# Kernel optimization log

Measured on AMD Instinct MI355X. Metric: run time of the kernel, lower is better.

The kernel has to match this reference:

```python
import jax, jax.numpy as jnp
import numpy as np

B, D_IN, R, D_P, K, D_C, ITERS = 4096, 2048, 7, 128, 25, 16, 3


def _ln(x, g, b, eps=1e-5):
    m = jnp.mean(x, axis=-1, keepdims=True)
    v = jnp.var(x, axis=-1, keepdims=True)
    return (x - m) * jax.lax.rsqrt(v + eps) * g + b


def _squash(x):
    eps = 1e-6
    ns = jnp.sum(x * x, axis=-1, keepdims=True)
    scale = ns / jnp.maximum(1.0 + ns, eps)
    return scale * x / (jnp.sqrt(ns) + eps)


def setup_inputs() -> dict:
    key = jax.random.key(0)
    ks = jax.random.split(key, 8)
    f = lambda k, shp, s=0.02: (jax.random.normal(k, shp) * s).astype(jnp.float32)
    return {
        "z": jax.random.normal(ks[0], (B, D_IN), jnp.float32),
        "W_prim": f(ks[1], (D_IN, R * D_P)),
        "b_prim": jnp.zeros((R * D_P,), jnp.float32),
        "ln_a_g": jnp.ones((D_IN,), jnp.float32),
        "ln_a_b": jnp.zeros((D_IN,), jnp.float32),
        "W_act": f(ks[2], (D_IN, R)),
        "b_act": jnp.zeros((R,), jnp.float32),
        "w_caps": (np.sqrt(K / (D_P * R)).astype(np.float32)
                   * jax.random.normal(ks[3], (R, D_P, K, D_C))).astype(jnp.float32),
        "ln_c_g": jnp.ones((D_C,), jnp.float32),
        "ln_c_b": jnp.zeros((D_C,), jnp.float32),
        "beta_u": f(ks[4], (K,), 1.0),
        "ln_h_g": jnp.ones((R * D_C,), jnp.float32),
        "ln_h_b": jnp.zeros((R * D_C,), jnp.float32),
        "W_h1": f(ks[5], (R * D_C, 4 * R * D_C)),
        "b_h1": jnp.zeros((4 * R * D_C,), jnp.float32),
        "W_h2": f(ks[6], (4 * R * D_C, 1)),
        "b_h2": jnp.zeros((1,), jnp.float32),
    }


def reference(z, W_prim, b_prim, ln_a_g, ln_a_b, W_act, b_act, w_caps,
              ln_c_g, ln_c_b, beta_u, ln_h_g, ln_h_b, W_h1, b_h1, W_h2, b_h2):
    # primary capsules: [B, R, D_P] poses + [B, R] activations
    pose = _squash((z @ W_prim + b_prim).reshape(B, R, D_P))
    act = jnp.clip(jax.nn.sigmoid(_ln(z, ln_a_g, ln_a_b) @ W_act + b_act), 0.0, 1.0)

    # votes: [B, R, K, D_C]
    u = jnp.einsum('brd,rdkh->brkh', pose, w_caps)
    scale = 1.0 / np.sqrt(D_C).astype(np.float32)

    # iterative routing (EM/softmax-agreement style)
    q = jnp.full((B, R, K), 1.0 / K, dtype=z.dtype)
    class_pose = None
    for _ in range(ITERS):
        wts = q * act[:, :, None]                               # [B,R,K]
        class_pose = _ln(jnp.einsum('brk,brkh->bkh', wts, u), ln_c_g, ln_c_b)
        agree = jnp.einsum('bkh,brkh->brk', class_pose, u) * scale
        q = jax.nn.softmax(agree, axis=-1)

    class_act = jax.nn.sigmoid(beta_u[None, :] + jnp.einsum('brk,br->bk', q, act))
    route_class_emb = q[..., None] * u                          # [B,R,K,D_C]

    # concat per-route interaction vectors -> [B, K, R*D_C]
    class_embed = jnp.transpose(route_class_emb, (0, 2, 1, 3)).reshape(B, K, R * D_C)
    h = jax.nn.gelu(_ln(class_embed, ln_h_g, ln_h_b) @ W_h1 + b_h1, approximate=False)
    logits = (h @ W_h2 + b_h2)[..., 0]                          # [B, K]

    return (logits, class_embed, class_pose, class_act, q, pose, act, route_class_emb)
```

## Files before the change

### kernel.cpp

```cpp
#include <hip/hip_runtime.h>
#include <cstddef>

#define BB 4096
#define DIN 2048
#define RR 7
#define DP 128
#define KK 25
#define DC 16
#define NITERS 3
#define RKH (RR*KK*DC)
#define RK  (RR*KK)
#define KH  (KK*DC)
#define HD  (RR*DC)
#define H4  (4*HD)

typedef __attribute__((ext_vector_type(8))) short bf16x8;
typedef __attribute__((ext_vector_type(4))) float f32x4;

__device__ __forceinline__ unsigned pk_bf16(float a, float b) {
    union { float f; unsigned u; } xa, xb;
    xa.f = a; xb.f = b;
    unsigned ua = (xa.u + 0x7FFFu + ((xa.u >> 16) & 1u)) >> 16;
    unsigned ub = (xb.u + 0x7FFFu + ((xb.u >> 16) & 1u)) >> 16;
    return (ua & 0xFFFFu) | (ub << 16);
}

__device__ __forceinline__ float gelu_tanh(float x) {
    float x3 = x * x * x;
    float tt = 0.7978845608f * (x + 0.044715f * x3);
    float e = __expf(2.0f * tt);
    float th = 1.0f - 2.0f / (e + 1.0f);
    return 0.5f * x * (1.0f + th);
}

__global__ __launch_bounds__(256) void transpose_cvt_kernel(
    const float* __restrict__ src, unsigned short* __restrict__ dst, int RS, int CS)
{
    __shared__ float T[64][65];
    int r0 = blockIdx.x * 64, c0 = blockIdx.y * 64;
    size_t bo = (size_t)blockIdx.z * RS * CS;
    src += bo; dst += bo;
    int t = threadIdx.x;
    for (int s = t; s < 64 * 16; s += 256) {
        int row = s >> 4, c4 = s & 15;
        int gr = r0 + row, gc = c0 + c4 * 4;
        float4 v = make_float4(0.f, 0.f, 0.f, 0.f);
        if (gr < RS && gc < CS) v = *(const float4*)(src + (size_t)gr * CS + gc);
        T[row][c4 * 4 + 0] = v.x; T[row][c4 * 4 + 1] = v.y;
        T[row][c4 * 4 + 2] = v.z; T[row][c4 * 4 + 3] = v.w;
    }
    __syncthreads();
    for (int s = t; s < 64 * 16; s += 256) {
        int col = s >> 4, r4 = s & 15;
        int gc = c0 + col, gr = r0 + r4 * 4;
        if (gc < CS && gr + 3 < RS) {
            unsigned lo = pk_bf16(T[r4 * 4 + 0][col], T[r4 * 4 + 1][col]);
            unsigned hi = pk_bf16(T[r4 * 4 + 2][col], T[r4 * 4 + 3][col]);
            *(uint2*)(dst + (size_t)gc * RS + gr) = make_uint2(lo, hi);
        }
    }
}

__global__ __launch_bounds__(256) void act_kernel(
    const float* __restrict__ z, const float* __restrict__ g, const float* __restrict__ bb,
    const float* __restrict__ Wa, const float* __restrict__ ba,
    float* __restrict__ act_out)
{
    int b = blockIdx.x;
    int t = threadIdx.x;
    __shared__ float zs[DIN];
    __shared__ float ws1[4], ws2[4];
    __shared__ float wr[4][RR];
    const float* zr = z + (size_t)b * DIN;
    float s = 0.f, s2 = 0.f;
    for (int i = t; i < DIN; i += 256) {
        float v = zr[i]; zs[i] = v; s += v; s2 += v * v;
    }
    for (int off = 32; off; off >>= 1) { s += __shfl_down(s, off); s2 += __shfl_down(s2, off); }
    int w = t >> 6, lane = t & 63;
    if (lane == 0) { ws1[w] = s; ws2[w] = s2; }
    __syncthreads();
    s  = ws1[0] + ws1[1] + ws1[2] + ws1[3];
    s2 = ws2[0] + ws2[1] + ws2[2] + ws2[3];
    float mean = s * (1.0f / DIN);
    float var  = s2 * (1.0f / DIN) - mean * mean;
    float rstd = rsqrtf(var + 1e-5f);
    float acc[RR];
#pragma unroll
    for (int r = 0; r < RR; ++r) acc[r] = 0.f;
    for (int i = t; i < DIN; i += 256) {
        float y = (zs[i] - mean) * rstd * g[i] + bb[i];
#pragma unroll
        for (int r = 0; r < RR; ++r) acc[r] += y * Wa[i * RR + r];
    }
    for (int off = 32; off; off >>= 1) {
#pragma unroll
        for (int r = 0; r < RR; ++r) acc[r] += __shfl_down(acc[r], off);
    }
    if (lane == 0) {
#pragma unroll
        for (int r = 0; r < RR; ++r) wr[w][r] = acc[r];
    }
    __syncthreads();
    if (t < RR) {
        float v = wr[0][t] + wr[1][t] + wr[2][t] + wr[3][t] + ba[t];
        float sg = 1.0f / (1.0f + expf(-v));
        sg = fminf(fmaxf(sg, 0.0f), 1.0f);
        act_out[(size_t)b * RR + t] = sg;
    }
}

__global__ __launch_bounds__(256) void pose_mfma(
    const float* __restrict__ z, const unsigned short* __restrict__ WpT,
    const float* __restrict__ bp, float* __restrict__ pose_out)
{
    __shared__ __align__(16) unsigned short As[128 * 40];
    __shared__ __align__(16) unsigned short Bs[128 * 40];
    __shared__ float sq[2][128];
    int m0 = blockIdx.x * 128, r = blockIdx.y, t = threadIdx.x;
    int n0 = r * DP;
    int w = t >> 6, l = t & 63;
    int lrow = l & 15, koff = l >> 4;
    int rbase = (w >> 1) * 64, cbase = (w & 1) * 64;
    f32x4 acc[4][4];
#pragma unroll
    for (int i = 0; i < 4; ++i)
#pragma unroll
        for (int j = 0; j < 4; ++j) acc[i][j] = 0.0f;
    for (int kt = 0; kt < DIN; kt += 32) {
#pragma unroll
        for (int q = 0; q < 4; ++q) {
            int s = t + 256 * q;
            int row = s >> 3, k4 = s & 7;
            float4 v = *(const float4*)(z + (size_t)(m0 + row) * DIN + kt + k4 * 4);
            *(uint2*)(As + row * 40 + k4 * 4) = make_uint2(pk_bf16(v.x, v.y), pk_bf16(v.z, v.w));
        }
#pragma unroll
        for (int q = 0; q < 2; ++q) {
            int s = t + 256 * q;
            int col = s >> 2, k8 = s & 3;
            uint4 v = *(const uint4*)(WpT + (size_t)(n0 + col) * DIN + kt + k8 * 8);
            *(uint4*)(Bs + col * 40 + k8 * 8) = v;
        }
        __syncthreads();
        bf16x8 a[4], b[4];
#pragma unroll
        for (int i = 0; i < 4; ++i)
            a[i] = *(const bf16x8*)(As + (rbase + i * 16 + lrow) * 40 + koff * 8);
#pragma unroll
        for (int j = 0; j < 4; ++j)
            b[j] = *(const bf16x8*)(Bs + (cbase + j * 16 + lrow) * 40 + koff * 8);
#pragma unroll
        for (int i = 0; i < 4; ++i)
#pragma unroll
            for (int j = 0; j < 4; ++j)
                acc[i][j] = __builtin_amdgcn_mfma_f32_16x16x32_bf16(a[i], b[j], acc[i][j], 0, 0, 0);
        __syncthreads();
    }
    float bpv[4];
#pragma unroll
    for (int j = 0; j < 4; ++j) bpv[j] = bp[n0 + cbase + j * 16 + lrow];
    float ns_[4][4];
#pragma unroll
    for (int i = 0; i < 4; ++i)
#pragma unroll
        for (int reg = 0; reg < 4; ++reg) {
            float ss = 0.f;
#pragma unroll
            for (int j = 0; j < 4; ++j) {
                float x = acc[i][j][reg] + bpv[j];
                acc[i][j][reg] = x;
                ss += x * x;
            }
            ss += __shfl_xor(ss, 1); ss += __shfl_xor(ss, 2);
            ss += __shfl_xor(ss, 4); ss += __shfl_xor(ss, 8);
            ns_[i][reg] = ss;
        }
    if (lrow == 0) {
#pragma unroll
        for (int i = 0; i < 4; ++i)
#pragma unroll
            for (int reg = 0; reg < 4; ++reg)
                sq[w & 1][rbase + i * 16 + koff * 4 + reg] = ns_[i][reg];
    }
    __syncthreads();
#pragma unroll
    for (int i = 0; i < 4; ++i)
#pragma unroll
        for (int reg = 0; reg < 4; ++reg) {
            int rl = rbase + i * 16 + koff * 4 + reg;
            float ns = sq[0][rl] + sq[1][rl];
            float factor = (ns / fmaxf(1.0f + ns, 1e-6f)) / (sqrtf(ns) + 1e-6f);
            size_t rowbase = ((size_t)(m0 + rl) * RR + r) * DP;
#pragma unroll
            for (int j = 0; j < 4; ++j)
                pose_out[rowbase + cbase + j * 16 + lrow] = acc[i][j][reg] * factor;
        }
}

__global__ __launch_bounds__(256) void votes_mfma(
    const float* __restrict__ pose, const unsigned short* __restrict__ wcT,
    float* __restrict__ u_out)
{
    __shared__ __align__(16) unsigned short As[128 * 152];
    __shared__ __align__(16) unsigned short Bs[80 * 152];
    int m0 = blockIdx.x * 128, r = blockIdx.y, n0 = blockIdx.z * 80;
    int t = threadIdx.x;
    int w = t >> 6, l = t & 63;
    int lrow = l & 15, koff = l >> 4;
    int rbase = w * 32;
#pragma unroll
    for (int q = 0; q < 16; ++q) {
        int s = t + 256 * q;
        int row = s >> 5, k4 = s & 31;
        float4 v = *(const float4*)(pose + ((size_t)(m0 + row) * RR + r) * DP + k4 * 4);
        *(uint2*)(As + row * 152 + k4 * 4) = make_uint2(pk_bf16(v.x, v.y), pk_bf16(v.z, v.w));
    }
    const unsigned short* wr_ = wcT + (size_t)r * KH * DP;
#pragma unroll
    for (int q = 0; q < 5; ++q) {
        int s = t + 256 * q;
        int col = s >> 4, k8 = s & 15;
        uint4 v = *(const uint4*)(wr_ + (size_t)(n0 + col) * DP + k8 * 8);
        *(uint4*)(Bs + col * 152 + k8 * 8) = v;
    }
    __syncthreads();
    f32x4 acc[2][5];
#pragma unroll
    for (int i = 0; i < 2; ++i)
#pragma unroll
        for (int j = 0; j < 5; ++j) acc[i][j] = 0.0f;
#pragma unroll
    for (int ks = 0; ks < 4; ++ks) {
        bf16x8 a[2], b[5];
#pragma unroll
        for (int i = 0; i < 2; ++i)
            a[i] = *(const bf16x8*)(As + (rbase + i * 16 + lrow) * 152 + ks * 32 + koff * 8);
#pragma unroll
        for (int j = 0; j < 5; ++j)
            b[j] = *(const bf16x8*)(Bs + (j * 16 + lrow) * 152 + ks * 32 + koff * 8);
#pragma unroll
        for (int i = 0; i < 2; ++i)
#pragma unroll
            for (int j = 0; j < 5; ++j)
                acc[i][j] = __builtin_amdgcn_mfma_f32_16x16x32_bf16(a[i], b[j], acc[i][j], 0, 0, 0);
    }
#pragma unroll
    for (int i = 0; i < 2; ++i)
#pragma unroll
        for (int reg = 0; reg < 4; ++reg) {
            int row = m0 + rbase + i * 16 + koff * 4 + reg;
            size_t base = ((size_t)row * RR + r) * KH + n0;
#pragma unroll
            for (int j = 0; j < 5; ++j)
                u_out[base + j * 16 + lrow] = acc[i][j][reg];
        }
}

__global__ __launch_bounds__(64) void routing_kernel(
    const float* __restrict__ u_in, const float* __restrict__ act_in,
    const float* __restrict__ lncg, const float* __restrict__ lncb,
    const float* __restrict__ beta_u,
    float* __restrict__ q_out, float* __restrict__ cp_out,
    float* __restrict__ ca_out, float* __restrict__ rce_out,
    float* __restrict__ ce_out)
{
    __shared__ __align__(16) float U[RKH];
    __shared__ float Q[RK];
    __shared__ float CP[KH];
    __shared__ float AG[RK];
    __shared__ float A7[RR];
    int b = blockIdx.x, t = threadIdx.x;
    const float4* u4 = (const float4*)(u_in + (size_t)b * RKH);
    float4* U4 = (float4*)U;
    for (int p = t; p < RKH / 4; p += 64) U4[p] = u4[p];
    if (t < RR) A7[t] = act_in[(size_t)b * RR + t];
    for (int p = t; p < RK; p += 64) Q[p] = 1.0f / KK;
    __syncthreads();
    for (int it = 0; it < NITERS; ++it) {
        for (int p = t; p < KH; p += 64) {
            int k = p / DC;
            float s = 0.f;
#pragma unroll
            for (int r = 0; r < RR; ++r) s += Q[r * KK + k] * A7[r] * U[r * KH + p];
            CP[p] = s;
        }
        __syncthreads();
        if (t < KK) {
            float m = 0.f;
#pragma unroll
            for (int h = 0; h < DC; ++h) m += CP[t * DC + h];
            m *= (1.0f / DC);
            float v = 0.f;
#pragma unroll
            for (int h = 0; h < DC; ++h) { float d = CP[t * DC + h] - m; v += d * d; }
            v *= (1.0f / DC);
            float rstd = rsqrtf(v + 1e-5f);
#pragma unroll
            for (int h = 0; h < DC; ++h)
                CP[t * DC + h] = (CP[t * DC + h] - m) * rstd * lncg[h] + lncb[h];
        }
        __syncthreads();
        for (int p = t; p < RK; p += 64) {
            int r = p / KK, k = p % KK;
            float s = 0.f;
#pragma unroll
            for (int h = 0; h < DC; ++h) s += CP[k * DC + h] * U[r * KH + k * DC + h];
            AG[p] = s * 0.25f;
        }
        __syncthreads();
        if (t < RR) {
            float mx = -1e30f;
            for (int k = 0; k < KK; ++k) mx = fmaxf(mx, AG[t * KK + k]);
            float e[KK], sum = 0.f;
            for (int k = 0; k < KK; ++k) { e[k] = expf(AG[t * KK + k] - mx); sum += e[k]; }
            float inv = 1.0f / sum;
            for (int k = 0; k < KK; ++k) Q[t * KK + k] = e[k] * inv;
        }
        __syncthreads();
    }
    if (t < KK) {
        float s = 0.f;
#pragma unroll
        for (int r = 0; r < RR; ++r) s += Q[r * KK + t] * A7[r];
        ca_out[(size_t)b * KK + t] = 1.0f / (1.0f + expf(-(beta_u[t] + s)));
    }
    for (int p = t; p < RK; p += 64) q_out[(size_t)b * RK + p] = Q[p];
    for (int p = t; p < KH; p += 64) cp_out[(size_t)b * KH + p] = CP[p];
    float4* rce4 = (float4*)(rce_out + (size_t)b * RKH);
    float4* ce4  = (float4*)ce_out;
    for (int p4 = t; p4 < RKH / 4; p4 += 64) {
        int base = p4 * 4;
        int r  = base / KH;
        int k  = (base % KH) / DC;
        int h0 = base % DC;
        float qv = Q[r * KK + k];
        float4 uv = U4[p4];
        float4 rv = make_float4(qv * uv.x, qv * uv.y, qv * uv.z, qv * uv.w);
        rce4[p4] = rv;
        size_t ci = ((size_t)b * RKH + (size_t)k * HD + (size_t)r * DC + h0) >> 2;
        ce4[ci] = rv;
    }
}

__global__ __launch_bounds__(256) void head_mfma(
    const float* __restrict__ ce, const float* __restrict__ g, const float* __restrict__ bb,
    const unsigned short* __restrict__ W1T, const float* __restrict__ b1,
    const float* __restrict__ W2, const float* __restrict__ b2,
    float* __restrict__ logits)
{
    __shared__ __align__(16) unsigned short As[128 * 152];
    __shared__ __align__(16) char pool[64 * 116 * 4];
    __shared__ float gbuf[HD], bbuf[HD];
    float* scr = (float*)pool;
    unsigned short* Bs = (unsigned short*)pool;
    unsigned* As32 = (unsigned*)As;
    unsigned* Bs32 = (unsigned*)Bs;
    int row0 = blockIdx.x * 128;
    int t = threadIdx.x;
    int w = t >> 6, l = t & 63;
    int lrow = l & 15, koff = l >> 4;
    if (t < HD) { gbuf[t] = g[t]; bbuf[t] = bb[t]; }
    for (int p = 0; p < 2; ++p) {
        for (int s = t; s < 64 * 28; s += 256) {
            int row = s / 28, q4 = s % 28;
            float4 v = *(const float4*)(ce + (size_t)(row0 + p * 64 + row) * HD + q4 * 4);
            *(float4*)(scr + row * 116 + q4 * 4) = v;
        }
        __syncthreads();
        {
            int tq = t & 3, row = t >> 2;
            float s1 = 0.f, s2 = 0.f;
            const float* rp = scr + row * 116 + tq * 28;
            for (int q = 0; q < 28; ++q) { float v = rp[q]; s1 += v; s2 += v * v; }
            s1 += __shfl_xor(s1, 1); s2 += __shfl_xor(s2, 1);
            s1 += __shfl_xor(s1, 2); s2 += __shfl_xor(s2, 2);
            float mean = s1 * (1.0f / HD);
            float var  = s2 * (1.0f / HD) - mean * mean;
            float rstd = rsqrtf(var + 1e-5f);
            int grow = p * 64 + row;
            for (int j = 0; j < 14; ++j) {
                int k = tq * 28 + 2 * j;
                float a = (rp[2 * j]     - mean) * rstd * gbuf[k]     + bbuf[k];
                float bv = (rp[2 * j + 1] - mean) * rstd * gbuf[k + 1] + bbuf[k + 1];
                As32[grow * 76 + tq * 14 + j] = pk_bf16(a, bv);
            }
        }
        __syncthreads();
    }
    for (int s = t; s < 128 * 8; s += 256) { int row = s >> 3; As32[row * 76 + 56 + (s & 7)] = 0; }
    for (int s = t; s < 64 * 8;  s += 256) { int col = s >> 3; Bs32[col * 76 + 56 + (s & 7)] = 0; }
    int rbase = w * 32;
    float logitAcc[2][4];
#pragma unroll
    for (int i = 0; i < 2; ++i)
#pragma unroll
        for (int reg = 0; reg < 4; ++reg) logitAcc[i][reg] = 0.f;
    for (int nc = 0; nc < 7; ++nc) {
        __syncthreads();
        for (int s = t; s < 64 * 14; s += 256) {
            int col = s / 14, k4 = s % 14;
            uint4 v = *(const uint4*)(W1T + (size_t)(nc * 64 + col) * HD + k4 * 8);
            *(uint4*)(Bs + col * 152 + k4 * 8) = v;
        }
        __syncthreads();
        f32x4 acc[2][4];
#pragma unroll
        for (int i = 0; i < 2; ++i)
#pragma unroll
            for (int j = 0; j < 4; ++j) acc[i][j] = 0.0f;
#pragma unroll
        for (int ks = 0; ks < 4; ++ks) {
            bf16x8 a[2], b[4];
#pragma unroll
            for (int i = 0; i < 2; ++i)
                a[i] = *(const bf16x8*)(As + (rbase + i * 16 + lrow) * 152 + ks * 32 + koff * 8);
#pragma unroll
            for (int j = 0; j < 4; ++j)
                b[j] = *(const bf16x8*)(Bs + (j * 16 + lrow) * 152 + ks * 32 + koff * 8);
#pragma unroll
            for (int i = 0; i < 2; ++i)
#pragma unroll
                for (int j = 0; j < 4; ++j)
                    acc[i][j] = __builtin_amdgcn_mfma_f32_16x16x32_bf16(a[i], b[j], acc[i][j], 0, 0, 0);
        }
        float b1v[4], w2v[4];
#pragma unroll
        for (int j = 0; j < 4; ++j) {
            b1v[j] = b1[nc * 64 + j * 16 + lrow];
            w2v[j] = W2[nc * 64 + j * 16 + lrow];
        }
#pragma unroll
        for (int i = 0; i < 2; ++i)
#pragma unroll
            for (int reg = 0; reg < 4; ++reg) {
                float sum = 0.f;
#pragma unroll
                for (int j = 0; j < 4; ++j) {
                    float x = acc[i][j][reg] + b1v[j];
                    sum += gelu_tanh(x) * w2v[j];
                }
                logitAcc[i][reg] += sum;
            }
    }
#pragma unroll
    for (int i = 0; i < 2; ++i)
#pragma unroll
        for (int reg = 0; reg < 4; ++reg) {
            float v = logitAcc[i][reg];
            v += __shfl_xor(v, 1); v += __shfl_xor(v, 2);
            v += __shfl_xor(v, 4); v += __shfl_xor(v, 8);
            logitAcc[i][reg] = v;
        }
    if (lrow == 0) {
        float b2v = b2[0];
#pragma unroll
        for (int i = 0; i < 2; ++i)
#pragma unroll
            for (int reg = 0; reg < 4; ++reg)
                logits[row0 + rbase + i * 16 + koff * 4 + reg] = logitAcc[i][reg] + b2v;
    }
}

__global__ __launch_bounds__(256) void pose_kernel(
    const float* __restrict__ z, const float* __restrict__ Wp, const float* __restrict__ bp,
    float* __restrict__ pose_out)
{
    __shared__ __align__(16) float As[64 * 36];
    __shared__ __align__(16) float Bs[32 * 128];
    int m0 = blockIdx.x * 64;
    int r  = blockIdx.y;
    int n0 = r * DP;
    int t  = threadIdx.x;
    int rg = t >> 5;
    int cg = t & 31;
    float acc[8][4] = {};
    for (int kt = 0; kt < DIN; kt += 32) {
#pragma unroll
        for (int q = 0; q < 2; ++q) {
            int s = t * 2 + q;
            int row = s >> 3, k4 = s & 7;
            float4 v = *(const float4*)(z + (size_t)(m0 + row) * DIN + kt + k4 * 4);
            *(float4*)(As + row * 36 + k4 * 4) = v;
        }
#pragma unroll
        for (int q = 0; q < 4; ++q) {
            int s = t + 256 * q;
            int row = s >> 5, c4 = s & 31;
            float4 v = *(const float4*)(Wp + (size_t)(kt + row) * (RR * DP) + n0 + c4 * 4);
            *(float4*)(Bs + row * 128 + c4 * 4) = v;
        }
        __syncthreads();
#pragma unroll
        for (int kk = 0; kk < 32; ++kk) {
            float4 bv = *(const float4*)(Bs + kk * 128 + cg * 4);
#pragma unroll
            for (int j = 0; j < 8; ++j) {
                float a = As[(rg * 8 + j) * 36 + kk];
                acc[j][0] += a * bv.x; acc[j][1] += a * bv.y;
                acc[j][2] += a * bv.z; acc[j][3] += a * bv.w;
            }
        }
        __syncthreads();
    }
    float bi0 = bp[n0 + cg * 4], bi1 = bp[n0 + cg * 4 + 1];
    float bi2 = bp[n0 + cg * 4 + 2], bi3 = bp[n0 + cg * 4 + 3];
#pragma unroll
    for (int j = 0; j < 8; ++j) {
        float x0 = acc[j][0] + bi0, x1 = acc[j][1] + bi1;
        float x2 = acc[j][2] + bi2, x3 = acc[j][3] + bi3;
        float ns = x0 * x0 + x1 * x1 + x2 * x2 + x3 * x3;
        for (int off = 1; off < 32; off <<= 1) ns += __shfl_xor(ns, off);
        float factor = (ns / fmaxf(1.0f + ns, 1e-6f)) / (sqrtf(ns) + 1e-6f);
        int row = m0 + rg * 8 + j;
        float4 o = make_float4(x0 * factor, x1 * factor, x2 * factor, x3 * factor);
        *(float4*)(pose_out + ((size_t)row * RR + r) * DP + cg * 4) = o;
    }
}

__global__ __launch_bounds__(256) void votes_kernel(
    const float* __restrict__ pose, const float* __restrict__ wc,
    float* __restrict__ u_out)
{
    __shared__ float As[64 * 129];
    __shared__ __align__(16) float Bs[64 * 80];
    int m0 = blockIdx.x * 64;
    int r  = blockIdx.y;
    int n0 = blockIdx.z * 80;
    int t  = threadIdx.x;
    const size_t wbase = (size_t)r * DP * KH;
#pragma unroll
    for (int q = 0; q < 8; ++q) {
        int s = t + 256 * q;
        int row = s >> 5, d4 = s & 31;
        float4 v = *(const float4*)(pose + ((size_t)(m0 + row) * RR + r) * DP + d4 * 4);
        As[row * 129 + d4 * 4 + 0] = v.x;
        As[row * 129 + d4 * 4 + 1] = v.y;
        As[row * 129 + d4 * 4 + 2] = v.z;
        As[row * 129 + d4 * 4 + 3] = v.w;
    }
    int m4 = t >> 4, n5 = t & 15;
    float acc[4][5];
#pragma unroll
    for (int i = 0; i < 4; ++i)
#pragma unroll
        for (int j = 0; j < 5; ++j) acc[i][j] = 0.f;
    for (int kt = 0; kt < DP; kt += 64) {
        __syncthreads();
#pragma unroll
        for (int q = 0; q < 5; ++q) {
            int s = t + 256 * q;
            int d = s / 20, c4 = s % 20;
            float4 v = *(const float4*)(wc + wbase + (size_t)(kt + d) * KH + n0 + c4 * 4);
            *(float4*)(Bs + d * 80 + c4 * 4) = v;
        }
        __syncthreads();
#pragma unroll 4
        for (int dd = 0; dd < 64; ++dd) {
            int d = kt + dd;
            float b_[5];
#pragma unroll
            for (int j = 0; j < 5; ++j) b_[j] = Bs[dd * 80 + n5 * 5 + j];
#pragma unroll
            for (int i = 0; i < 4; ++i) {
                float a = As[(m4 * 4 + i) * 129 + d];
#pragma unroll
                for (int j = 0; j < 5; ++j) acc[i][j] += a * b_[j];
            }
        }
    }
#pragma unroll
    for (int i = 0; i < 4; ++i) {
        int row = m0 + m4 * 4 + i;
        size_t base = ((size_t)row * RR + r) * KH + n0 + n5 * 5;
#pragma unroll
        for (int j = 0; j < 5; ++j) u_out[base + j] = acc[i][j];
    }
}

__global__ __launch_bounds__(256) void head_kernel(
    const float* __restrict__ ce, const float* __restrict__ g, const float* __restrict__ bb,
    const float* __restrict__ W1, const float* __restrict__ b1,
    const float* __restrict__ W2, const float* __restrict__ b2,
    float* __restrict__ logits)
{
    __shared__ __align__(16) float Y[64 * HD];
    __shared__ float Wc[HD * 64];
    __shared__ float Lg[64];
    int row0 = blockIdx.x * 64;
    int t = threadIdx.x;
    for (int s = t; s < 64 * HD; s += 256) Y[s] = ce[(size_t)row0 * HD + s];
    __syncthreads();
    if (t < 64) {
        float m = 0.f;
        for (int i = 0; i < HD; ++i) m += Y[t * HD + i];
        m *= (1.0f / HD);
        float v = 0.f;
        for (int i = 0; i < HD; ++i) { float d = Y[t * HD + i] - m; v += d * d; }
        v *= (1.0f / HD);
        float rstd = rsqrtf(v + 1e-5f);
        for (int i = 0; i < HD; ++i) Y[t * HD + i] = (Y[t * HD + i] - m) * rstd * g[i] + bb[i];
    }
    int rg = t >> 4;
    int cg = t & 15;
    float accRow[4] = {0.f, 0.f, 0.f, 0.f};
    for (int c0 = 0; c0 < H4; c0 += 64) {
        __syncthreads();
        for (int s = t; s < HD * 64; s += 256) {
            int i = s >> 6, c = s & 63;
            Wc[i * 64 + c] = W1[(size_t)i * H4 + c0 + c];
        }
        __syncthreads();
        float b1v[4], w2v[4];
#pragma unroll
        for (int c = 0; c < 4; ++c) { b1v[c] = b1[c0 + cg * 4 + c]; w2v[c] = W2[c0 + cg * 4 + c]; }
        float s_[4][4];
#pragma unroll
        for (int rr = 0; rr < 4; ++rr)
#pragma unroll
            for (int c = 0; c < 4; ++c) s_[rr][c] = b1v[c];
        for (int i4 = 0; i4 < HD / 4; ++i4) {
            float4 y4[4];
#pragma unroll
            for (int rr = 0; rr < 4; ++rr)
                y4[rr] = *(const float4*)(Y + (rg * 4 + rr) * HD + i4 * 4);
#pragma unroll
            for (int is = 0; is < 4; ++is) {
                float w_[4];
#pragma unroll
                for (int c = 0; c < 4; ++c) w_[c] = Wc[(i4 * 4 + is) * 64 + cg * 4 + c];
#pragma unroll
                for (int rr = 0; rr < 4; ++rr) {
                    float yv = (is == 0) ? y4[rr].x : (is == 1) ? y4[rr].y : (is == 2) ? y4[rr].z : y4[rr].w;
#pragma unroll
                    for (int c = 0; c < 4; ++c) s_[rr][c] += yv * w_[c];
                }
            }
        }
#pragma unroll
        for (int rr = 0; rr < 4; ++rr) {
#pragma unroll
            for (int c = 0; c < 4; ++c) {
                float x = s_[rr][c];
                float ge = 0.5f * x * (1.0f + erff(x * 0.70710678118654752440f));
                accRow[rr] += ge * w2v[c];
            }
        }
    }
#pragma unroll
    for (int rr = 0; rr < 4; ++rr) {
        float v = accRow[rr];
        v += __shfl_xor(v, 1); v += __shfl_xor(v, 2);
        v += __shfl_xor(v, 4); v += __shfl_xor(v, 8);
        if (cg == 0) Lg[rg * 4 + rr] = v;
    }
    __syncthreads();
    if (t < 64) logits[row0 + t] = Lg[t] + b2[0];
}

extern "C" void kernel_launch(void* const* d_in, const int* in_sizes, int n_in,
                              void* d_out, int out_size, void* d_ws, size_t ws_size,
                              hipStream_t stream) {
    const float* z    = (const float*)d_in[0];
    const float* Wp   = (const float*)d_in[1];
    const float* bp   = (const float*)d_in[2];
    const float* lnag = (const float*)d_in[3];
    const float* lnab = (const float*)d_in[4];
    const float* Wa   = (const float*)d_in[5];
    const float* ba   = (const float*)d_in[6];
    const float* wc   = (const float*)d_in[7];
    const float* lncg = (const float*)d_in[8];
    const float* lncb = (const float*)d_in[9];
    const float* beta = (const float*)d_in[10];
    const float* lnhg = (const float*)d_in[11];
    const float* lnhb = (const float*)d_in[12];
    const float* W1   = (const float*)d_in[13];
    const float* b1   = (const float*)d_in[14];
    const float* W2   = (const float*)d_in[15];
    const float* b2   = (const float*)d_in[16];

    float* out = (float*)d_out;
    float* o_logits = out;
    float* o_ce   = o_logits + (size_t)BB * KK;
    float* o_cp   = o_ce   + (size_t)BB * KK * HD;
    float* o_ca   = o_cp   + (size_t)BB * KK * DC;
    float* o_q    = o_ca   + (size_t)BB * KK;
    float* o_pose = o_q    + (size_t)BB * RK;
    float* o_act  = o_pose + (size_t)BB * RR * DP;
    float* o_rce  = o_act  + (size_t)BB * RR;

    const size_t WPT_ELE = (size_t)(RR * DP) * DIN;
    const size_t W1T_ELE = (size_t)H4 * HD;
    const size_t WCT_ELE = (size_t)RR * KH * DP;
    const size_t WS_NEED = (WPT_ELE + W1T_ELE + WCT_ELE) * sizeof(unsigned short);
    unsigned short* WpT = (unsigned short*)d_ws;
    unsigned short* W1T = WpT + WPT_ELE;
    unsigned short* wcT = W1T + W1T_ELE;

    hipLaunchKernelGGL(act_kernel, dim3(BB), dim3(256), 0, stream,
                       z, lnag, lnab, Wa, ba, o_act);

    if (ws_size >= WS_NEED) {
        hipLaunchKernelGGL(transpose_cvt_kernel, dim3(DIN / 64, (RR * DP) / 64, 1), dim3(256), 0, stream,
                           Wp, WpT, DIN, RR * DP);
        hipLaunchKernelGGL(transpose_cvt_kernel, dim3(2, 7, 1), dim3(256), 0, stream,
                           W1, W1T, HD, H4);
        hipLaunchKernelGGL(transpose_cvt_kernel, dim3(2, 7, RR), dim3(256), 0, stream,
                           wc, wcT, DP, KH);
        hipLaunchKernelGGL(pose_mfma, dim3(BB / 128, RR), dim3(256), 0, stream,
                           z, WpT, bp, o_pose);
        hipLaunchKernelGGL(votes_mfma, dim3(BB / 128, RR, 5), dim3(256), 0, stream,
                           o_pose, wcT, o_rce);
        hipLaunchKernelGGL(routing_kernel, dim3(BB), dim3(64), 0, stream,
                           o_rce, o_act, lncg, lncb, beta, o_q, o_cp, o_ca, o_rce, o_ce);
        hipLaunchKernelGGL(head_mfma, dim3(BB * KK / 128), dim3(256), 0, stream,
                           o_ce, lnhg, lnhb, W1T, b1, W2, b2, o_logits);
    } else {
        hipLaunchKernelGGL(pose_kernel, dim3(BB / 64, RR), dim3(256), 0, stream,
                           z, Wp, bp, o_pose);
        hipLaunchKernelGGL(votes_kernel, dim3(BB / 64, RR, 5), dim3(256), 0, stream,
                           o_pose, wc, o_rce);
        hipLaunchKernelGGL(routing_kernel, dim3(BB), dim3(64), 0, stream,
                           o_rce, o_act, lncg, lncb, beta, o_q, o_cp, o_ca, o_rce, o_ce);
        hipLaunchKernelGGL(head_kernel, dim3(BB * KK / 64), dim3(256), 0, stream,
                           o_ce, lnhg, lnhb, W1, b1, W2, b2, o_logits);
    }
}
```

Baseline: 387.4 us.

## Pre-swizzle W1 into MFMA fragment order and stage it once via LDS DMA

A new prep kernel writes W1 as bf16 laid out in MFMA fragment order, zero-padded to K=128. The head kernel loads the whole 448x128 weight block into LDS once with global_load_lds, removing the per-chunk barriers and the strided LDS loads. It also computes LayerNorm straight from registers into fragment-ordered A tiles held in registers, and caches b1/W2 in LDS. In exchange LDS use per block grows a lot (about 150KB), which lowers occupancy to one block per CU.

```diff
diff --git a/kernel.cpp b/kernel.cpp
--- a/kernel.cpp
+++ b/kernel.cpp
@@ -59,6 +59,21 @@
             *(uint2*)(dst + (size_t)gc * RS + gr) = make_uint2(lo, hi);
         }
     }
+}
+
+__global__ __launch_bounds__(256) void w1_frag_kernel(
+    const float* __restrict__ W1, unsigned short* __restrict__ W1F)
+{
+    int d = blockIdx.x * 256 + threadIdx.x;
+    int e2 = d & 3;
+    int lane = (d >> 2) & 63;
+    int fid = d >> 8;
+    int j = fid & 3, ks = (fid >> 2) & 3, nc = fid >> 4;
+    int col = nc * 64 + j * 16 + (lane & 15);
+    int k = ks * 32 + (lane >> 4) * 8 + e2 * 2;
+    float a = (k < HD)     ? W1[(size_t)k * H4 + col]       : 0.f;
+    float b = (k + 1 < HD) ? W1[(size_t)(k + 1) * H4 + col] : 0.f;
+    ((unsigned*)W1F)[d] = pk_bf16(a, b);
 }
 
 __global__ __launch_bounds__(256) void act_kernel(
@@ -345,65 +360,95 @@
 
 __global__ __launch_bounds__(256) void head_mfma(
     const float* __restrict__ ce, const float* __restrict__ g, const float* __restrict__ bb,
-    const unsigned short* __restrict__ W1T, const float* __restrict__ b1,
+    const unsigned short* __restrict__ W1F, const float* __restrict__ b1,
     const float* __restrict__ W2, const float* __restrict__ b2,
     float* __restrict__ logits)
 {
-    __shared__ __align__(16) unsigned short As[128 * 152];
-    __shared__ __align__(16) char pool[64 * 116 * 4];
-    __shared__ float gbuf[HD], bbuf[HD];
-    float* scr = (float*)pool;
-    unsigned short* Bs = (unsigned short*)pool;
-    unsigned* As32 = (unsigned*)As;
-    unsigned* Bs32 = (unsigned*)Bs;
+    __shared__ __align__(16) unsigned short As[128 * 128];
+    __shared__ __align__(16) unsigned short Bs[448 * 128];
+    __shared__ float LB1[H4];
+    __shared__ float LW2[H4];
     int row0 = blockIdx.x * 128;
     int t = threadIdx.x;
     int w = t >> 6, l = t & 63;
     int lrow = l & 15, koff = l >> 4;
-    if (t < HD) { gbuf[t] = g[t]; bbuf[t] = bb[t]; }
-    for (int p = 0; p < 2; ++p) {
-        for (int s = t; s < 64 * 28; s += 256) {
-            int row = s / 28, q4 = s % 28;
-            float4 v = *(const float4*)(ce + (size_t)(row0 + p * 64 + row) * HD + q4 * 4);
-            *(float4*)(scr + row * 116 + q4 * 4) = v;
-        }
-        __syncthreads();
-        {
-            int tq = t & 3, row = t >> 2;
-            float s1 = 0.f, s2 = 0.f;
-            const float* rp = scr + row * 116 + tq * 28;
-            for (int q = 0; q < 28; ++q) { float v = rp[q]; s1 += v; s2 += v * v; }
-            s1 += __shfl_xor(s1, 1); s2 += __shfl_xor(s2, 1);
-            s1 += __shfl_xor(s1, 2); s2 += __shfl_xor(s2, 2);
-            float mean = s1 * (1.0f / HD);
-            float var  = s2 * (1.0f / HD) - mean * mean;
-            float rstd = rsqrtf(var + 1e-5f);
-            int grow = p * 64 + row;
-            for (int j = 0; j < 14; ++j) {
-                int k = tq * 28 + 2 * j;
-                float a = (rp[2 * j]     - mean) * rstd * gbuf[k]     + bbuf[k];
-                float bv = (rp[2 * j + 1] - mean) * rstd * gbuf[k + 1] + bbuf[k + 1];
-                As32[grow * 76 + tq * 14 + j] = pk_bf16(a, bv);
-            }
-        }
-        __syncthreads();
-    }
-    for (int s = t; s < 128 * 8; s += 256) { int row = s >> 3; As32[row * 76 + 56 + (s & 7)] = 0; }
-    for (int s = t; s < 64 * 8;  s += 256) { int col = s >> 3; Bs32[col * 76 + 56 + (s & 7)] = 0; }
-    int rbase = w * 32;
+
+#pragma unroll
+    for (int q = 0; q < 28; ++q) {
+        int chunk = w * 28 + q;
+        __builtin_amdgcn_global_load_lds(
+            (const __attribute__((address_space(1))) unsigned int*)(const void*)(W1F + (size_t)chunk * 512 + l * 8),
+            (__attribute__((address_space(3))) unsigned int*)(void*)(Bs + chunk * 512),
+            16, 0, 0);
+    }
+    for (int s = t; s < H4; s += 256) { LB1[s] = b1[s]; LW2[s] = W2[s]; }
+
+    {
+        int row = t >> 1, half = t & 1;
+        const float* rp = ce + (size_t)(row0 + row) * HD + half * 56;
+        float4 v[14];
+#pragma unroll
+        for (int m = 0; m < 14; ++m) v[m] = *(const float4*)(rp + m * 4);
+        float s1 = 0.f, s2 = 0.f;
+#pragma unroll
+        for (int m = 0; m < 14; ++m) {
+            s1 += v[m].x + v[m].y + v[m].z + v[m].w;
+            s2 += v[m].x * v[m].x + v[m].y * v[m].y + v[m].z * v[m].z + v[m].w * v[m].w;
+        }
+        s1 += __shfl_xor(s1, 1); s2 += __shfl_xor(s2, 1);
+        float mean = s1 * (1.0f / HD);
+        float var  = s2 * (1.0f / HD) - mean * mean;
+        float rstd = rsqrtf(var + 1e-5f);
+        int lr = row & 15, rt = row >> 4;
+#pragma unroll
+        for (int j = 0; j < 7; ++j) {
+            float4 gl0 = *(const float4*)(g  + half * 56 + j * 8);
+            float4 gl1 = *(const float4*)(g  + half * 56 + j * 8 + 4);
+            float4 bl0 = *(const float4*)(bb + half * 56 + j * 8);
+            float4 bl1 = *(const float4*)(bb + half * 56 + j * 8 + 4);
+            float4 x0 = v[j * 2], x1 = v[j * 2 + 1];
+            float y0 = (x0.x - mean) * rstd * gl0.x + bl0.x;
+            float y1 = (x0.y - mean) * rstd * gl0.y + bl0.y;
+            float y2 = (x0.z - mean) * rstd * gl0.z + bl0.z;
+            float y3 = (x0.w - mean) * rstd * gl0.w + bl0.w;
+            float y4 = (x1.x - mean) * rstd * gl1.x + bl1.x;
+            float y5 = (x1.y - mean) * rstd * gl1.y + bl1.y;
+            float y6 = (x1.z - mean) * rstd * gl1.z + bl1.z;
+            float y7 = (x1.w - mean) * rstd * gl1.w + bl1.w;
+            int k8 = half * 7 + j;
+            int ks = k8 >> 2, ko = k8 & 3;
+            unsigned* dst = (unsigned*)(As + (size_t)((rt * 4 + ks) * 64 + ko * 16 + lr) * 8);
+            dst[0] = pk_bf16(y0, y1); dst[1] = pk_bf16(y2, y3);
+            dst[2] = pk_bf16(y4, y5); dst[3] = pk_bf16(y6, y7);
+        }
+        if (half) {
+            uint4 z4 = make_uint4(0, 0, 0, 0);
+            *(uint4*)(As + (size_t)((rt * 4 + 3) * 64 + 2 * 16 + lr) * 8) = z4;
+            *(uint4*)(As + (size_t)((rt * 4 + 3) * 64 + 3 * 16 + lr) * 8) = z4;
+        }
+    }
+    __syncthreads();
+
+    bf16x8 af[2][4];
+#pragma unroll
+    for (int i = 0; i < 2; ++i)
+#pragma unroll
+        for (int ks = 0; ks < 4; ++ks)
+            af[i][ks] = *(const bf16x8*)(As + (size_t)(((w * 2 + i) * 4 + ks) * 64 + l) * 8);
+
     float logitAcc[2][4];
 #pragma unroll
     for (int i = 0; i < 2; ++i)
 #pragma unroll
         for (int reg = 0; reg < 4; ++reg) logitAcc[i][reg] = 0.f;
+
     for (int nc = 0; nc < 7; ++nc) {
-        __syncthreads();
-        for (int s = t; s < 64 * 14; s += 256) {
-            int col = s / 14, k4 = s % 14;
-            uint4 v = *(const uint4*)(W1T + (size_t)(nc * 64 + col) * HD + k4 * 8);
-            *(uint4*)(Bs + col * 152 + k4 * 8) = v;
-        }
-        __syncthreads();
+        float b1v[4], w2v[4];
+#pragma unroll
+        for (int j = 0; j < 4; ++j) {
+            b1v[j] = LB1[nc * 64 + j * 16 + lrow];
+            w2v[j] = LW2[nc * 64 + j * 16 + lrow];
+        }
         f32x4 acc[2][4];
 #pragma unroll
         for (int i = 0; i < 2; ++i)
@@ -411,24 +456,15 @@
             for (int j = 0; j < 4; ++j) acc[i][j] = 0.0f;
 #pragma unroll
         for (int ks = 0; ks < 4; ++ks) {
-            bf16x8 a[2], b[4];
+            bf16x8 b[4];
+#pragma unroll
+            for (int j = 0; j < 4; ++j)
+                b[j] = *(const bf16x8*)(Bs + (size_t)(((nc * 4 + ks) * 4 + j) * 64 + l) * 8);
 #pragma unroll
             for (int i = 0; i < 2; ++i)
-                a[i] = *(const bf16x8*)(As + (rbase + i * 16 + lrow) * 152 + ks * 32 + koff * 8);
-#pragma unroll
-            for (int j = 0; j < 4; ++j)
-                b[j] = *(const bf16x8*)(Bs + (j * 16 + lrow) * 152 + ks * 32 + koff * 8);
-#pragma unroll
-            for (int i = 0; i < 2; ++i)
 #pragma unroll
                 for (int j = 0; j < 4; ++j)
-                    acc[i][j] = __builtin_amdgcn_mfma_f32_16x16x32_bf16(a[i], b[j], acc[i][j], 0, 0, 0);
-        }
-        float b1v[4], w2v[4];
-#pragma unroll
-        for (int j = 0; j < 4; ++j) {
-            b1v[j] = b1[nc * 64 + j * 16 + lrow];
-            w2v[j] = W2[nc * 64 + j * 16 + lrow];
+                    acc[i][j] = __builtin_amdgcn_mfma_f32_16x16x32_bf16(af[i][ks], b[j], acc[i][j], 0, 0, 0);
         }
 #pragma unroll
         for (int i = 0; i < 2; ++i)
@@ -447,10 +483,10 @@
     for (int i = 0; i < 2; ++i)
 #pragma unroll
         for (int reg = 0; reg < 4; ++reg) {
-            float v = logitAcc[i][reg];
-            v += __shfl_xor(v, 1); v += __shfl_xor(v, 2);
-            v += __shfl_xor(v, 4); v += __shfl_xor(v, 8);
-            logitAcc[i][reg] = v;
+            float vv = logitAcc[i][reg];
+            vv += __shfl_xor(vv, 1); vv += __shfl_xor(vv, 2);
+            vv += __shfl_xor(vv, 4); vv += __shfl_xor(vv, 8);
+            logitAcc[i][reg] = vv;
         }
     if (lrow == 0) {
         float b2v = b2[0];
@@ -458,7 +494,7 @@
         for (int i = 0; i < 2; ++i)
 #pragma unroll
             for (int reg = 0; reg < 4; ++reg)
-                logits[row0 + rbase + i * 16 + koff * 4 + reg] = logitAcc[i][reg] + b2v;
+                logits[row0 + w * 32 + i * 16 + koff * 4 + reg] = logitAcc[i][reg] + b2v;
     }
 }
 
@@ -690,12 +726,12 @@
     float* o_rce  = o_act  + (size_t)BB * RR;
 
     const size_t WPT_ELE = (size_t)(RR * DP) * DIN;
-    const size_t W1T_ELE = (size_t)H4 * HD;
+    const size_t W1F_ELE = (size_t)H4 * 128;
     const size_t WCT_ELE = (size_t)RR * KH * DP;
-    const size_t WS_NEED = (WPT_ELE + W1T_ELE + WCT_ELE) * sizeof(unsigned short);
+    const size_t WS_NEED = (WPT_ELE + W1F_ELE + WCT_ELE) * sizeof(unsigned short);
     unsigned short* WpT = (unsigned short*)d_ws;
-    unsigned short* W1T = WpT + WPT_ELE;
-    unsigned short* wcT = W1T + W1T_ELE;
+    unsigned short* W1F = WpT + WPT_ELE;
+    unsigned short* wcT = W1F + W1F_ELE;
 
     hipLaunchKernelGGL(act_kernel, dim3(BB), dim3(256), 0, stream,
                        z, lnag, lnab, Wa, ba, o_act);
@@ -703,8 +739,8 @@
     if (ws_size >= WS_NEED) {
         hipLaunchKernelGGL(transpose_cvt_kernel, dim3(DIN / 64, (RR * DP) / 64, 1), dim3(256), 0, stream,
                            Wp, WpT, DIN, RR * DP);
-        hipLaunchKernelGGL(transpose_cvt_kernel, dim3(2, 7, 1), dim3(256), 0, stream,
-                           W1, W1T, HD, H4);
+        hipLaunchKernelGGL(w1_frag_kernel, dim3(112), dim3(256), 0, stream,
+                           W1, W1F);
         hipLaunchKernelGGL(transpose_cvt_kernel, dim3(2, 7, RR), dim3(256), 0, stream,
                            wc, wcT, DP, KH);
         hipLaunchKernelGGL(pose_mfma, dim3(BB / 128, RR), dim3(256), 0, stream,
@@ -714,7 +750,7 @@
         hipLaunchKernelGGL(routing_kernel, dim3(BB), dim3(64), 0, stream,
                            o_rce, o_act, lncg, lncb, beta, o_q, o_cp, o_ca, o_rce, o_ce);
         hipLaunchKernelGGL(head_mfma, dim3(BB * KK / 128), dim3(256), 0, stream,
-                           o_ce, lnhg, lnhb, W1T, b1, W2, b2, o_logits);
+                           o_ce, lnhg, lnhb, W1F, b1, W2, b2, o_logits);
     } else {
         hipLaunchKernelGGL(pose_kernel, dim3(BB / 64, RR), dim3(256), 0, stream,
                            z, Wp, bp, o_pose);
```

After: 382.6 us. Within noise of the previous version (-1.2%).
